# Optimization experiments

Measured on AMD Instinct MI355X. Metric: run time of the kernel, lower is better.

Reference implementation:

```python
import jax, jax.numpy as jnp
import numpy as np

N, D = 8192, 1024
NUM_CLASSES = 200
NUM_BATCHES = 128  # stands in for len(train_loader)


def setup_inputs() -> dict:
    key = jax.random.key(0)
    k1, k2, k3, k4 = jax.random.split(key, 4)
    return {
        "reconstructed_image_features": jax.random.normal(k1, (N, D), dtype=jnp.float32),
        "semantic_embeddings": jax.random.normal(k2, (N, D), dtype=jnp.float32),
        "residual_output": jax.random.normal(k3, (N, D), dtype=jnp.float32),
        "labels": jax.random.randint(k4, (N,), 0, NUM_CLASSES, dtype=jnp.int64),
    }


def reference(reconstructed_image_features, semantic_embeddings, residual_output, labels):
    # Normalize rows -> pairwise cosine similarity via one Gram matmul.
    z = semantic_embeddings
    eps = 1e-8  # matches torch CosineSimilarity eps
    zn = z / jnp.maximum(jnp.linalg.norm(z, axis=1, keepdims=True), eps)
    S = zn @ zn.T                      # [N, N] cosine similarities
    E = jnp.exp(S)                     # exp(cos_sim) for every pair

    same = labels[:, None] == labels[None, :]          # same-class mask
    offdiag = ~jnp.eye(S.shape[0], dtype=bool)         # torch.equal skip == skip i==j

    row_same = jnp.sum(jnp.where(same & offdiag, E, 0.0), axis=1)  # [N]
    row_diff = jnp.sum(jnp.where(~same, E, 0.0), axis=1)           # [N]

    seg_same = jax.ops.segment_sum(row_same, labels, num_segments=NUM_CLASSES)
    seg_diff = jax.ops.segment_sum(row_diff, labels, num_segments=NUM_CLASSES)
    counts = jax.ops.segment_sum(jnp.ones_like(row_same), labels, num_segments=NUM_CLASSES)

    present = counts > 0  # original only iterates over labels present in the batch
    safe_same = jnp.where(present, seg_same, 1.0)
    safe_diff = jnp.where(present, seg_diff, 1.0)
    per_label = jnp.where(present, jnp.log(safe_same / safe_diff), 0.0)

    return jnp.sum(per_label) / NUM_BATCHES
```

## Files before the change

### kernel.cpp

```cpp
#include <hip/hip_runtime.h>
#include <hip/hip_bf16.h>
#include <stdint.h>

#define N_ROWS 8192
#define DIM 1024
#define NUM_CLS 200
#define NT 64
#define NSUP 10
#define GRID_BLOCKS (NSUP * 256)

typedef __attribute__((ext_vector_type(8))) short bf16x8;
typedef __attribute__((ext_vector_type(4))) float f32x4;

__device__ __forceinline__ ushort f2bf(float f) {
    __hip_bfloat16 h = __float2bfloat16(f);
    return *reinterpret_cast<ushort*>(&h);
}

__global__ __launch_bounds__(256) void normalize_kernel(const float* __restrict__ z,
                                                        ushort* __restrict__ zn) {
    const int row = blockIdx.x * 4 + (threadIdx.x >> 6);
    const int lane = threadIdx.x & 63;
    const float4 v = reinterpret_cast<const float4*>(z + (size_t)row * DIM)[lane];
    float ss = v.x * v.x + v.y * v.y + v.z * v.z + v.w * v.w;
    #pragma unroll
    for (int off = 1; off < 64; off <<= 1) ss += __shfl_xor(ss, off);
    const float inv = 1.0f / fmaxf(sqrtf(ss), 1e-8f);
    ushort4 o;
    o.x = f2bf(v.x * inv);
    o.y = f2bf(v.y * inv);
    o.z = f2bf(v.z * inv);
    o.w = f2bf(v.w * inv);
    reinterpret_cast<ushort4*>(zn + (size_t)row * DIM)[lane] = o;
}

__global__ __launch_bounds__(256) void gram_kernel(const ushort* __restrict__ zn,
                                                   const int* __restrict__ labels,
                                                   float* __restrict__ row_same,
                                                   float* __restrict__ row_diff) {
    constexpr int SBi[NSUP] = {0, 0, 0, 0, 1, 1, 1, 2, 2, 3};
    constexpr int SBj[NSUP] = {0, 1, 2, 3, 1, 2, 3, 2, 3, 3};

    const int st = blockIdx.x >> 8;
    const int p = blockIdx.x & 255;
    const int xcd = p & 7;
    const int idx = p >> 3;
    const int bi_local = (xcd >> 1) * 4 + (idx >> 3);
    const int bj_local = (xcd & 1) * 8 + (idx & 7);
    const int bi = SBi[st] * 16 + bi_local;
    const int bj = SBj[st] * 16 + bj_local;
    if (bi > bj) return;
    const bool diag = (bi == bj);

    __shared__ ushort sA[128 * 64];
    __shared__ ushort sB[128 * 64];
    __shared__ int labR[128], labC[128];

    const int r0 = bi * 128, c0 = bj * 128;
    const int t = threadIdx.x;
    const int lane = t & 63, wv = t >> 6;
    const int wr = wv >> 1, wc = wv & 1;

    if (t < 128) labR[t] = labels[r0 + t];
    else labC[t - 128] = labels[c0 + (t - 128)];

    f32x4 acc[4][4];
    #pragma unroll
    for (int m = 0; m < 4; m++)
        #pragma unroll
        for (int n = 0; n < 4; n++) acc[m][n] = (f32x4){0.f, 0.f, 0.f, 0.f};

    const int lrow = lane >> 3;
    const int lcol = lane & 7;

    for (int kt = 0; kt < DIM; kt += 64) {
        #pragma unroll
        for (int c = 0; c < 4; c++) {
            const int rowT = wv * 32 + c * 8 + lrow;
            const ushort* gA = zn + (size_t)(r0 + rowT) * DIM + kt + lcol * 8;
            __builtin_amdgcn_global_load_lds(
                (const __attribute__((address_space(1))) uint32_t*)gA,
                (__attribute__((address_space(3))) uint32_t*)&sA[rowT * 64 + lcol * 8],
                16, 0, 0);
            const ushort* gB = zn + (size_t)(c0 + rowT) * DIM + kt + lcol * 8;
            __builtin_amdgcn_global_load_lds(
                (const __attribute__((address_space(1))) uint32_t*)gB,
                (__attribute__((address_space(3))) uint32_t*)&sB[rowT * 64 + lcol * 8],
                16, 0, 0);
        }
        __syncthreads();
        #pragma unroll
        for (int ks = 0; ks < 2; ks++) {
            const int kof = ks * 32 + (lane >> 4) * 8;
            bf16x8 af[4], bfr[4];
            #pragma unroll
            for (int m = 0; m < 4; m++)
                af[m] = *reinterpret_cast<const bf16x8*>(
                    &sA[(wr * 64 + m * 16 + (lane & 15)) * 64 + kof]);
            #pragma unroll
            for (int n = 0; n < 4; n++)
                bfr[n] = *reinterpret_cast<const bf16x8*>(
                    &sB[(wc * 64 + n * 16 + (lane & 15)) * 64 + kof]);
            #pragma unroll
            for (int m = 0; m < 4; m++)
                #pragma unroll
                for (int n = 0; n < 4; n++)
                    acc[m][n] = __builtin_amdgcn_mfma_f32_16x16x32_bf16(
                        af[m], bfr[n], acc[m][n], 0, 0, 0);
        }
        __syncthreads();
    }

    float rs[4][4], rd[4][4];
    float cs[4], cd[4];
    #pragma unroll
    for (int m = 0; m < 4; m++)
        #pragma unroll
        for (int q = 0; q < 4; q++) { rs[m][q] = 0.f; rd[m][q] = 0.f; }

    #pragma unroll
    for (int n = 0; n < 4; n++) {
        const int jj = wc * 64 + n * 16 + (lane & 15);
        const int j = c0 + jj;
        const int lj = labC[jj];
        float csn = 0.f, cdn = 0.f;
        #pragma unroll
        for (int m = 0; m < 4; m++) {
            #pragma unroll
            for (int q = 0; q < 4; q++) {
                const int ii = wr * 64 + m * 16 + (lane >> 4) * 4 + q;
                const float e = __expf(acc[m][n][q]);
                const bool same = (labR[ii] == lj);
                if (diag) {
                    if (r0 + ii != j) {
                        if (same) rs[m][q] += e; else rd[m][q] += e;
                    }
                } else {
                    if (same) { rs[m][q] += e; csn += e; }
                    else      { rd[m][q] += e; cdn += e; }
                }
            }
        }
        cs[n] = csn; cd[n] = cdn;
    }

    #pragma unroll
    for (int m = 0; m < 4; m++) {
        #pragma unroll
        for (int q = 0; q < 4; q++) {
            float vs = rs[m][q], vd = rd[m][q];
            #pragma unroll
            for (int off = 1; off < 16; off <<= 1) {
                vs += __shfl_xor(vs, off);
                vd += __shfl_xor(vd, off);
            }
            if ((lane & 15) == 0) {
                const int i = r0 + wr * 64 + m * 16 + (lane >> 4) * 4 + q;
                atomicAdd(&row_same[i], vs);
                atomicAdd(&row_diff[i], vd);
            }
        }
    }

    if (!diag) {
        #pragma unroll
        for (int n = 0; n < 4; n++) {
            float vs = cs[n], vd = cd[n];
            vs += __shfl_xor(vs, 16); vd += __shfl_xor(vd, 16);
            vs += __shfl_xor(vs, 32); vd += __shfl_xor(vd, 32);
            if (lane < 16) {
                const int j = c0 + wc * 64 + n * 16 + lane;
                atomicAdd(&row_same[j], vs);
                atomicAdd(&row_diff[j], vd);
            }
        }
    }
}

__global__ __launch_bounds__(256) void class_sum_kernel(const int* __restrict__ labels,
                                                        const float* __restrict__ row_same,
                                                        const float* __restrict__ row_diff,
                                                        float* __restrict__ cls_same,
                                                        float* __restrict__ cls_diff,
                                                        int* __restrict__ cls_cnt) {
    __shared__ float ls[NUM_CLS], ld_[NUM_CLS];
    __shared__ int lc[NUM_CLS];
    const int t = threadIdx.x;
    for (int c = t; c < NUM_CLS; c += 256) { ls[c] = 0.f; ld_[c] = 0.f; lc[c] = 0; }
    __syncthreads();
    const int r = blockIdx.x * 256 + t;
    if (r < N_ROWS) {
        const int l = labels[r];
        atomicAdd(&ls[l], row_same[r]);
        atomicAdd(&ld_[l], row_diff[r]);
        atomicAdd(&lc[l], 1);
    }
    __syncthreads();
    for (int c = t; c < NUM_CLS; c += 256) {
        if (lc[c] > 0) {
            atomicAdd(&cls_same[c], ls[c]);
            atomicAdd(&cls_diff[c], ld_[c]);
            atomicAdd(&cls_cnt[c], lc[c]);
        }
    }
}

__global__ __launch_bounds__(256) void final_kernel(const float* __restrict__ cls_same,
                                                    const float* __restrict__ cls_diff,
                                                    const int* __restrict__ cls_cnt,
                                                    float* __restrict__ out) {
    const int t = threadIdx.x;
    float p = 0.f;
    if (t < NUM_CLS && cls_cnt[t] > 0) p = logf(cls_same[t] / cls_diff[t]);
    #pragma unroll
    for (int off = 1; off < 64; off <<= 1) p += __shfl_xor(p, off);
    __shared__ float wsum[4];
    if ((t & 63) == 0) wsum[t >> 6] = p;
    __syncthreads();
    if (t == 0) out[0] = (wsum[0] + wsum[1] + wsum[2] + wsum[3]) / 128.0f;
}

extern "C" void kernel_launch(void* const* d_in, const int* in_sizes, int n_in,
                              void* d_out, int out_size, void* d_ws, size_t ws_size,
                              hipStream_t stream) {
    const float* z = (const float*)d_in[1];
    const int* labels = (const int*)d_in[3];

    ushort* zn = (ushort*)d_ws;
    char* p = (char*)d_ws + (size_t)N_ROWS * DIM * 2;
    float* row_same = (float*)p;                 p += N_ROWS * sizeof(float);
    float* row_diff = (float*)p;                 p += N_ROWS * sizeof(float);
    float* cls_same = (float*)p;                 p += 256 * sizeof(float);
    float* cls_diff = (float*)p;                 p += 256 * sizeof(float);
    int*   cls_cnt  = (int*)p;

    hipMemsetAsync(row_same, 0,
                   (2 * N_ROWS + 2 * 256) * sizeof(float) + 256 * sizeof(int),
                   stream);

    normalize_kernel<<<N_ROWS / 4, 256, 0, stream>>>(z, zn);

    gram_kernel<<<GRID_BLOCKS, 256, 0, stream>>>(zn, labels, row_same, row_diff);

    class_sum_kernel<<<N_ROWS / 256, 256, 0, stream>>>(labels, row_same, row_diff,
                                                       cls_same, cls_diff, cls_cnt);
    final_kernel<<<1, 256, 0, stream>>>(cls_same, cls_diff, cls_cnt, (float*)d_out);
}
```

Before: 283.2 us.

## Use 256x256 tiles with double-buffered LDS, swizzle, and 512-thread blocks

Rewrites the Gram kernel to compute 256x256 output tiles per 512-thread block with 8 waves, BK=32, double-buffered shared memory and an XOR-style swizzle on the LDS layout. Loads for the next k-slice are issued before computing on the current one, and MFMA issue runs at raised wave priority. Larger tiles halve global reads per FLOP and the prefetch overlaps loads with math. In exchange there are fewer blocks (640, half skipped), one block per CU, higher register pressure and coarser load balance on the triangular grid.

```diff
diff --git a/kernel.cpp b/kernel.cpp
--- a/kernel.cpp
+++ b/kernel.cpp
@@ -5,9 +5,11 @@
 #define N_ROWS 8192
 #define DIM 1024
 #define NUM_CLS 200
-#define NT 64
+#define BM 256
+#define BK 32
+#define NT2 32
 #define NSUP 10
-#define GRID_BLOCKS (NSUP * 256)
+#define GRID_BLOCKS (NSUP * 64)
 
 typedef __attribute__((ext_vector_type(8))) short bf16x8;
 typedef __attribute__((ext_vector_type(4))) float f32x4;
@@ -34,130 +36,140 @@
     reinterpret_cast<ushort4*>(zn + (size_t)row * DIM)[lane] = o;
 }
 
-__global__ __launch_bounds__(256) void gram_kernel(const ushort* __restrict__ zn,
-                                                   const int* __restrict__ labels,
-                                                   float* __restrict__ row_same,
-                                                   float* __restrict__ row_diff) {
-    constexpr int SBi[NSUP] = {0, 0, 0, 0, 1, 1, 1, 2, 2, 3};
-    constexpr int SBj[NSUP] = {0, 1, 2, 3, 1, 2, 3, 2, 3, 3};
-
-    const int st = blockIdx.x >> 8;
-    const int p = blockIdx.x & 255;
+__global__ __launch_bounds__(512, 1) void gram_kernel(const ushort* __restrict__ zn,
+                                                      const int* __restrict__ labels,
+                                                      float* __restrict__ row_same,
+                                                      float* __restrict__ row_diff) {
+    constexpr int SBi[NSUP] = {0, 0, 1, 0, 1, 2, 0, 1, 2, 3};
+    constexpr int SBj[NSUP] = {0, 1, 1, 2, 2, 2, 3, 3, 3, 3};
+
+    const int st = blockIdx.x >> 6;
+    const int p = blockIdx.x & 63;
     const int xcd = p & 7;
     const int idx = p >> 3;
-    const int bi_local = (xcd >> 1) * 4 + (idx >> 3);
-    const int bj_local = (xcd & 1) * 8 + (idx & 7);
-    const int bi = SBi[st] * 16 + bi_local;
-    const int bj = SBj[st] * 16 + bj_local;
+    const int bi_l = (xcd & 3) * 2 + (idx >> 2);
+    const int bj_l = (xcd >> 2) * 4 + (idx & 3);
+    const int bi = SBi[st] * 8 + bi_l;
+    const int bj = SBj[st] * 8 + bj_l;
     if (bi > bj) return;
     const bool diag = (bi == bj);
 
-    __shared__ ushort sA[128 * 64];
-    __shared__ ushort sB[128 * 64];
-    __shared__ int labR[128], labC[128];
-
-    const int r0 = bi * 128, c0 = bj * 128;
+    const int r0 = bi * BM, c0 = bj * BM;
     const int t = threadIdx.x;
     const int lane = t & 63, wv = t >> 6;
-    const int wr = wv >> 1, wc = wv & 1;
-
-    if (t < 128) labR[t] = labels[r0 + t];
-    else labC[t - 128] = labels[c0 + (t - 128)];
-
-    f32x4 acc[4][4];
-    #pragma unroll
-    for (int m = 0; m < 4; m++)
+    const int wr = wv >> 2, wc = wv & 3;
+
+    __shared__ ushort sA[2][BM * BK];
+    __shared__ ushort sB[2][BM * BK];
+
+    f32x4 acc[8][4];
+    #pragma unroll
+    for (int m = 0; m < 8; m++)
         #pragma unroll
         for (int n = 0; n < 4; n++) acc[m][n] = (f32x4){0.f, 0.f, 0.f, 0.f};
 
-    const int lrow = lane >> 3;
-    const int lcol = lane & 7;
-
-    for (int kt = 0; kt < DIM; kt += 64) {
-        #pragma unroll
-        for (int c = 0; c < 4; c++) {
-            const int rowT = wv * 32 + c * 8 + lrow;
-            const ushort* gA = zn + (size_t)(r0 + rowT) * DIM + kt + lcol * 8;
+    auto stage = [&](int buf, int kt) {
+        #pragma unroll
+        for (int h = 0; h < 2; h++) {
+            const int c = h * 512 + t;
+            const int r = c >> 2;
+            const int sp = c & 3;
+            const int rr = (r + (r >> 2)) & 3;
+            const int s = (sp - rr) & 3;
+            const ushort* gA = zn + (size_t)(r0 + r) * DIM + kt + s * 8;
             __builtin_amdgcn_global_load_lds(
                 (const __attribute__((address_space(1))) uint32_t*)gA,
-                (__attribute__((address_space(3))) uint32_t*)&sA[rowT * 64 + lcol * 8],
+                (__attribute__((address_space(3))) uint32_t*)&sA[buf][c * 8],
                 16, 0, 0);
-            const ushort* gB = zn + (size_t)(c0 + rowT) * DIM + kt + lcol * 8;
+            const ushort* gB = zn + (size_t)(c0 + r) * DIM + kt + s * 8;
             __builtin_amdgcn_global_load_lds(
                 (const __attribute__((address_space(1))) uint32_t*)gB,
-                (__attribute__((address_space(3))) uint32_t*)&sB[rowT * 64 + lcol * 8],
+                (__attribute__((address_space(3))) uint32_t*)&sB[buf][c * 8],
                 16, 0, 0);
         }
+    };
+
+    stage(0, 0);
+    __syncthreads();
+
+    int cur = 0;
+    const int rbase = wr * 128 + (lane & 15);
+    const int cbase = wc * 64 + (lane & 15);
+    const int sidx = lane >> 4;
+
+    for (int it = 0; it < DIM / BK; ++it) {
+        if (it < DIM / BK - 1) stage(cur ^ 1, (it + 1) * BK);
+
+        bf16x8 a[4], b[4];
+        #pragma unroll
+        for (int x = 0; x < 4; x++) {
+            const int row = rbase + x * 16;
+            const int sp = (sidx + row + (row >> 2)) & 3;
+            a[x] = *reinterpret_cast<const bf16x8*>(&sA[cur][row * 32 + sp * 8]);
+            const int rowb = cbase + x * 16;
+            const int spb = (sidx + rowb + (rowb >> 2)) & 3;
+            b[x] = *reinterpret_cast<const bf16x8*>(&sB[cur][rowb * 32 + spb * 8]);
+        }
+        __builtin_amdgcn_s_setprio(1);
+        #pragma unroll
+        for (int m = 0; m < 4; m++)
+            #pragma unroll
+            for (int n = 0; n < 4; n++)
+                acc[m][n] = __builtin_amdgcn_mfma_f32_16x16x32_bf16(
+                    a[m], b[n], acc[m][n], 0, 0, 0);
+        __builtin_amdgcn_s_setprio(0);
+
+        #pragma unroll
+        for (int x = 0; x < 4; x++) {
+            const int row = rbase + (x + 4) * 16;
+            const int sp = (sidx + row + (row >> 2)) & 3;
+            a[x] = *reinterpret_cast<const bf16x8*>(&sA[cur][row * 32 + sp * 8]);
+        }
+        __builtin_amdgcn_s_setprio(1);
+        #pragma unroll
+        for (int m = 0; m < 4; m++)
+            #pragma unroll
+            for (int n = 0; n < 4; n++)
+                acc[m + 4][n] = __builtin_amdgcn_mfma_f32_16x16x32_bf16(
+                    a[m], b[n], acc[m + 4][n], 0, 0, 0);
+        __builtin_amdgcn_s_setprio(0);
+
         __syncthreads();
-        #pragma unroll
-        for (int ks = 0; ks < 2; ks++) {
-            const int kof = ks * 32 + (lane >> 4) * 8;
-            bf16x8 af[4], bfr[4];
-            #pragma unroll
-            for (int m = 0; m < 4; m++)
-                af[m] = *reinterpret_cast<const bf16x8*>(
-                    &sA[(wr * 64 + m * 16 + (lane & 15)) * 64 + kof]);
-            #pragma unroll
-            for (int n = 0; n < 4; n++)
-                bfr[n] = *reinterpret_cast<const bf16x8*>(
-                    &sB[(wc * 64 + n * 16 + (lane & 15)) * 64 + kof]);
-            #pragma unroll
-            for (int m = 0; m < 4; m++)
-                #pragma unroll
-                for (int n = 0; n < 4; n++)
-                    acc[m][n] = __builtin_amdgcn_mfma_f32_16x16x32_bf16(
-                        af[m], bfr[n], acc[m][n], 0, 0, 0);
-        }
-        __syncthreads();
-    }
-
-    float rs[4][4], rd[4][4];
-    float cs[4], cd[4];
-    #pragma unroll
-    for (int m = 0; m < 4; m++)
-        #pragma unroll
-        for (int q = 0; q < 4; q++) { rs[m][q] = 0.f; rd[m][q] = 0.f; }
-
-    #pragma unroll
-    for (int n = 0; n < 4; n++) {
-        const int jj = wc * 64 + n * 16 + (lane & 15);
-        const int j = c0 + jj;
-        const int lj = labC[jj];
-        float csn = 0.f, cdn = 0.f;
-        #pragma unroll
-        for (int m = 0; m < 4; m++) {
-            #pragma unroll
-            for (int q = 0; q < 4; q++) {
-                const int ii = wr * 64 + m * 16 + (lane >> 4) * 4 + q;
+        cur ^= 1;
+    }
+
+    int* labR = (int*)&sA[0][0];
+    int* labC = labR + 256;
+    if (t < 256) labR[t] = labels[r0 + t];
+    else labC[t - 256] = labels[c0 + (t - 256)];
+    __syncthreads();
+
+    float cs[4] = {0.f, 0.f, 0.f, 0.f}, cd[4] = {0.f, 0.f, 0.f, 0.f};
+    #pragma unroll
+    for (int m = 0; m < 8; m++) {
+        #pragma unroll
+        for (int q = 0; q < 4; q++) {
+            const int ii = wr * 128 + m * 16 + (lane >> 4) * 4 + q;
+            const int li = labR[ii];
+            float vs = 0.f, vd = 0.f;
+            #pragma unroll
+            for (int n = 0; n < 4; n++) {
+                const int jj = wc * 64 + n * 16 + (lane & 15);
                 const float e = __expf(acc[m][n][q]);
-                const bool same = (labR[ii] == lj);
-                if (diag) {
-                    if (r0 + ii != j) {
-                        if (same) rs[m][q] += e; else rd[m][q] += e;
-                    }
-                } else {
-                    if (same) { rs[m][q] += e; csn += e; }
-                    else      { rd[m][q] += e; cdn += e; }
+                const bool same = (li == labC[jj]);
+                if (!diag || ii != jj) {
+                    if (same) { vs += e; if (!diag) cs[n] += e; }
+                    else      { vd += e; if (!diag) cd[n] += e; }
                 }
             }
-        }
-        cs[n] = csn; cd[n] = cdn;
-    }
-
-    #pragma unroll
-    for (int m = 0; m < 4; m++) {
-        #pragma unroll
-        for (int q = 0; q < 4; q++) {
-            float vs = rs[m][q], vd = rd[m][q];
             #pragma unroll
             for (int off = 1; off < 16; off <<= 1) {
                 vs += __shfl_xor(vs, off);
                 vd += __shfl_xor(vd, off);
             }
             if ((lane & 15) == 0) {
-                const int i = r0 + wr * 64 + m * 16 + (lane >> 4) * 4 + q;
-                atomicAdd(&row_same[i], vs);
-                atomicAdd(&row_diff[i], vd);
+                atomicAdd(&row_same[r0 + ii], vs);
+                atomicAdd(&row_diff[r0 + ii], vd);
             }
         }
     }
@@ -240,7 +252,7 @@
 
     normalize_kernel<<<N_ROWS / 4, 256, 0, stream>>>(z, zn);
 
-    gram_kernel<<<GRID_BLOCKS, 256, 0, stream>>>(zn, labels, row_same, row_diff);
+    gram_kernel<<<GRID_BLOCKS, 512, 0, stream>>>(zn, labels, row_same, row_diff);
 
     class_sum_kernel<<<N_ROWS / 256, 256, 0, stream>>>(labels, row_same, row_diff,
                                                        cls_same, cls_diff, cls_cnt);
```

Result: faster. 266.8 us (-5.8%).

## Persistent XCD-chunked triangular tile scheduler with swizzled LDS layout

Applied to the files above, without the earlier changes.

Replaces the 2560-block launch, in which lower-triangle blocks exit early, with a persistent grid of 768 blocks. Each block loops over upper-triangular 128x128 tiles taken from a contiguous per-XCD chunk. It also XOR-style swizzles the LDS layout to reduce bank conflicts on the bf16x8 fragment reads, raises MFMA issue priority with s_setprio, and sets launch bounds to 3 blocks per CU. The aim is to remove empty-block launch overhead and tail imbalance and to improve L2 locality per XCD, at the cost of a serial tile-index decode loop and possible load imbalance across chunks.

```diff
diff --git a/kernel.cpp b/kernel.cpp
--- a/kernel.cpp
+++ b/kernel.cpp
@@ -5,9 +5,11 @@
 #define N_ROWS 8192
 #define DIM 1024
 #define NUM_CLS 200
-#define NT 64
-#define NSUP 10
-#define GRID_BLOCKS (NSUP * 256)
+#define NTT 64
+#define TILES (NTT * (NTT + 1) / 2)
+#define GRIDB 768
+#define CHUNK (TILES / 8)
+#define BSTR (GRIDB / 8)
 
 typedef __attribute__((ext_vector_type(8))) short bf16x8;
 typedef __attribute__((ext_vector_type(4))) float f32x4;
@@ -34,144 +36,137 @@
     reinterpret_cast<ushort4*>(zn + (size_t)row * DIM)[lane] = o;
 }
 
-__global__ __launch_bounds__(256) void gram_kernel(const ushort* __restrict__ zn,
-                                                   const int* __restrict__ labels,
-                                                   float* __restrict__ row_same,
-                                                   float* __restrict__ row_diff) {
-    constexpr int SBi[NSUP] = {0, 0, 0, 0, 1, 1, 1, 2, 2, 3};
-    constexpr int SBj[NSUP] = {0, 1, 2, 3, 1, 2, 3, 2, 3, 3};
-
-    const int st = blockIdx.x >> 8;
-    const int p = blockIdx.x & 255;
-    const int xcd = p & 7;
-    const int idx = p >> 3;
-    const int bi_local = (xcd >> 1) * 4 + (idx >> 3);
-    const int bj_local = (xcd & 1) * 8 + (idx & 7);
-    const int bi = SBi[st] * 16 + bi_local;
-    const int bj = SBj[st] * 16 + bj_local;
-    if (bi > bj) return;
-    const bool diag = (bi == bj);
-
+__global__ __launch_bounds__(256, 3) void gram_kernel(const ushort* __restrict__ zn,
+                                                      const int* __restrict__ labels,
+                                                      float* __restrict__ row_same,
+                                                      float* __restrict__ row_diff) {
     __shared__ ushort sA[128 * 64];
     __shared__ ushort sB[128 * 64];
     __shared__ int labR[128], labC[128];
 
-    const int r0 = bi * 128, c0 = bj * 128;
     const int t = threadIdx.x;
     const int lane = t & 63, wv = t >> 6;
     const int wr = wv >> 1, wc = wv & 1;
-
-    if (t < 128) labR[t] = labels[r0 + t];
-    else labC[t - 128] = labels[c0 + (t - 128)];
-
-    f32x4 acc[4][4];
+    const int lrow = lane & 15, lgrp = lane >> 4;
+    const int xcd = blockIdx.x & 7;
+    const int sub = blockIdx.x >> 3;
+
+    int gOff[4];
+    ushort* lA[4]; ushort* lB[4];
     #pragma unroll
-    for (int m = 0; m < 4; m++)
+    for (int i = 0; i < 4; i++) {
+        const int c = i * 256 + t;
+        const int r = c >> 3, sp = c & 7;
+        const int s = (sp - r - (r >> 3)) & 7;
+        gOff[i] = r * DIM + s * 8;
+        lA[i] = &sA[c * 8];
+        lB[i] = &sB[c * 8];
+    }
+
+    for (int w = xcd * CHUNK + sub; w < (xcd + 1) * CHUNK; w += BSTR) {
+        int rem = w, bi = 0, len = NTT;
+        while (rem >= len) { rem -= len; ++bi; --len; }
+        const int bj = bi + rem;
+        const bool diag = (bi == bj);
+        const int r0 = bi * 128, c0 = bj * 128;
+
+        __syncthreads();
+        if (t < 128) labR[t] = labels[r0 + t];
+        else labC[t - 128] = labels[c0 + (t - 128)];
+
+        f32x4 acc[4][4];
         #pragma unroll
-        for (int n = 0; n < 4; n++) acc[m][n] = (f32x4){0.f, 0.f, 0.f, 0.f};
-
-    const int lrow = lane >> 3;
-    const int lcol = lane & 7;
-
-    for (int kt = 0; kt < DIM; kt += 64) {
+        for (int m = 0; m < 4; m++)
+            #pragma unroll
+            for (int n = 0; n < 4; n++) acc[m][n] = (f32x4){0.f, 0.f, 0.f, 0.f};
+
+        const ushort* pa[4];
+        const ushort* pb[4];
         #pragma unroll
-        for (int c = 0; c < 4; c++) {
-            const int rowT = wv * 32 + c * 8 + lrow;
-            const ushort* gA = zn + (size_t)(r0 + rowT) * DIM + kt + lcol * 8;
-            __builtin_amdgcn_global_load_lds(
-                (const __attribute__((address_space(1))) uint32_t*)gA,
-                (__attribute__((address_space(3))) uint32_t*)&sA[rowT * 64 + lcol * 8],
-                16, 0, 0);
-            const ushort* gB = zn + (size_t)(c0 + rowT) * DIM + kt + lcol * 8;
-            __builtin_amdgcn_global_load_lds(
-                (const __attribute__((address_space(1))) uint32_t*)gB,
-                (__attribute__((address_space(3))) uint32_t*)&sB[rowT * 64 + lcol * 8],
-                16, 0, 0);
-        }
-        __syncthreads();
-        #pragma unroll
-        for (int ks = 0; ks < 2; ks++) {
-            const int kof = ks * 32 + (lane >> 4) * 8;
-            bf16x8 af[4], bfr[4];
-            #pragma unroll
-            for (int m = 0; m < 4; m++)
-                af[m] = *reinterpret_cast<const bf16x8*>(
-                    &sA[(wr * 64 + m * 16 + (lane & 15)) * 64 + kof]);
-            #pragma unroll
-            for (int n = 0; n < 4; n++)
-                bfr[n] = *reinterpret_cast<const bf16x8*>(
-                    &sB[(wc * 64 + n * 16 + (lane & 15)) * 64 + kof]);
-            #pragma unroll
-            for (int m = 0; m < 4; m++)
-                #pragma unroll
-                for (int n = 0; n < 4; n++)
-                    acc[m][n] = __builtin_amdgcn_mfma_f32_16x16x32_bf16(
-                        af[m], bfr[n], acc[m][n], 0, 0, 0);
-        }
-        __syncthreads();
-    }
-
-    float rs[4][4], rd[4][4];
-    float cs[4], cd[4];
-    #pragma unroll
-    for (int m = 0; m < 4; m++)
-        #pragma unroll
-        for (int q = 0; q < 4; q++) { rs[m][q] = 0.f; rd[m][q] = 0.f; }
-
-    #pragma unroll
-    for (int n = 0; n < 4; n++) {
-        const int jj = wc * 64 + n * 16 + (lane & 15);
-        const int j = c0 + jj;
-        const int lj = labC[jj];
-        float csn = 0.f, cdn = 0.f;
+        for (int i = 0; i < 4; i++) {
+            pa[i] = zn + (size_t)r0 * DIM + gOff[i];
+            pb[i] = zn + (size_t)c0 * DIM + gOff[i];
+        }
+
+        for (int it = 0; it < DIM / 64; ++it) {
+            #pragma unroll
+            for (int i = 0; i < 4; i++) {
+                __builtin_amdgcn_global_load_lds(
+                    (const __attribute__((address_space(1))) uint32_t*)pa[i],
+                    (__attribute__((address_space(3))) uint32_t*)lA[i], 16, 0, 0);
+                __builtin_amdgcn_global_load_lds(
+                    (const __attribute__((address_space(1))) uint32_t*)pb[i],
+                    (__attribute__((address_space(3))) uint32_t*)lB[i], 16, 0, 0);
+                pa[i] += 64; pb[i] += 64;
+            }
+            __syncthreads();
+
+            bf16x8 a[4][2], b[4][2];
+            #pragma unroll
+            for (int m = 0; m < 4; m++) {
+                const int Ra = wr * 64 + m * 16 + lrow;
+                const int Rb = wc * 64 + m * 16 + lrow;
+                #pragma unroll
+                for (int ks = 0; ks < 2; ks++) {
+                    const int spa = (ks * 4 + lgrp + Ra + (Ra >> 3)) & 7;
+                    const int spb = (ks * 4 + lgrp + Rb + (Rb >> 3)) & 7;
+                    a[m][ks] = *reinterpret_cast<const bf16x8*>(&sA[Ra * 64 + spa * 8]);
+                    b[m][ks] = *reinterpret_cast<const bf16x8*>(&sB[Rb * 64 + spb * 8]);
+                }
+            }
+            __builtin_amdgcn_s_setprio(1);
+            #pragma unroll
+            for (int ks = 0; ks < 2; ks++)
+                #pragma unroll
+                for (int m = 0; m < 4; m++)
+                    #pragma unroll
+                    for (int n = 0; n < 4; n++)
+                        acc[m][n] = __builtin_amdgcn_mfma_f32_16x16x32_bf16(
+                            a[m][ks], b[n][ks], acc[m][n], 0, 0, 0);
+            __builtin_amdgcn_s_setprio(0);
+            __syncthreads();
+        }
+
+        float cs[4] = {0.f, 0.f, 0.f, 0.f}, cd[4] = {0.f, 0.f, 0.f, 0.f};
         #pragma unroll
         for (int m = 0; m < 4; m++) {
             #pragma unroll
             for (int q = 0; q < 4; q++) {
-                const int ii = wr * 64 + m * 16 + (lane >> 4) * 4 + q;
-                const float e = __expf(acc[m][n][q]);
-                const bool same = (labR[ii] == lj);
-                if (diag) {
-                    if (r0 + ii != j) {
-                        if (same) rs[m][q] += e; else rd[m][q] += e;
+                const int ii = wr * 64 + m * 16 + lgrp * 4 + q;
+                const int li = labR[ii];
+                float vs = 0.f, vd = 0.f;
+                #pragma unroll
+                for (int n = 0; n < 4; n++) {
+                    const int jj = wc * 64 + n * 16 + lrow;
+                    const float e = __expf(acc[m][n][q]);
+                    const bool same = (li == labC[jj]);
+                    if (!diag || ii != jj) {
+                        if (same) { vs += e; if (!diag) cs[n] += e; }
+                        else      { vd += e; if (!diag) cd[n] += e; }
                     }
-                } else {
-                    if (same) { rs[m][q] += e; csn += e; }
-                    else      { rd[m][q] += e; cdn += e; }
-                }
-            }
-        }
-        cs[n] = csn; cd[n] = cdn;
-    }
-
-    #pragma unroll
-    for (int m = 0; m < 4; m++) {
-        #pragma unroll
-        for (int q = 0; q < 4; q++) {
-            float vs = rs[m][q], vd = rd[m][q];
-            #pragma unroll
-            for (int off = 1; off < 16; off <<= 1) {
-                vs += __shfl_xor(vs, off);
-                vd += __shfl_xor(vd, off);
-            }
-            if ((lane & 15) == 0) {
-                const int i = r0 + wr * 64 + m * 16 + (lane >> 4) * 4 + q;
-                atomicAdd(&row_same[i], vs);
-                atomicAdd(&row_diff[i], vd);
-            }
-        }
-    }
-
-    if (!diag) {
-        #pragma unroll
-        for (int n = 0; n < 4; n++) {
-            float vs = cs[n], vd = cd[n];
-            vs += __shfl_xor(vs, 16); vd += __shfl_xor(vd, 16);
-            vs += __shfl_xor(vs, 32); vd += __shfl_xor(vd, 32);
-            if (lane < 16) {
-                const int j = c0 + wc * 64 + n * 16 + lane;
-                atomicAdd(&row_same[j], vs);
-                atomicAdd(&row_diff[j], vd);
+                }
+                #pragma unroll
+                for (int off = 1; off < 16; off <<= 1) {
+                    vs += __shfl_xor(vs, off);
+                    vd += __shfl_xor(vd, off);
+                }
+                if (lrow == 0) {
+                    atomicAdd(&row_same[r0 + ii], vs);
+                    atomicAdd(&row_diff[r0 + ii], vd);
+                }
+            }
+        }
+        if (!diag) {
+            #pragma unroll
+            for (int n = 0; n < 4; n++) {
+                float vs = cs[n], vd = cd[n];
+                vs += __shfl_xor(vs, 16); vd += __shfl_xor(vd, 16);
+                vs += __shfl_xor(vs, 32); vd += __shfl_xor(vd, 32);
+                if (lane < 16) {
+                    const int j = c0 + wc * 64 + n * 16 + lane;
+                    atomicAdd(&row_same[j], vs);
+                    atomicAdd(&row_diff[j], vd);
+                }
             }
         }
     }
@@ -240,7 +235,7 @@
 
     normalize_kernel<<<N_ROWS / 4, 256, 0, stream>>>(z, zn);
 
-    gram_kernel<<<GRID_BLOCKS, 256, 0, stream>>>(zn, labels, row_same, row_diff);
+    gram_kernel<<<GRIDB, 256, 0, stream>>>(zn, labels, row_same, row_diff);
 
     class_sum_kernel<<<N_ROWS / 256, 256, 0, stream>>>(labels, row_same, row_diff,
                                                        cls_same, cls_diff, cls_cnt);
```

New measurement: 313.6 us. 1.11x slower.
